# Kernel optimization log

Measured on AMD Instinct MI355X. Metric: run time of the kernel, lower is better.

The kernel has to match this reference:

```python
import jax, jax.numpy as jnp
import numpy as np

E = 2048      # embed_dim = qk_dim = v_dim = proj_dim
H = 16        # n_head
D = 128       # head_dim
ROT = 64      # rotary_dim (partial rotary: ROT < D)
PAD = 50257   # pad_token_id in select_at_last_token
EPS = 1e-5    # layer_norm_epsilon


def _sincos(T):
    # fixed_pos_embedding (GPT-J style): [T, ROT//2] each
    inv_freq = 1.0 / (10000.0 ** (jnp.arange(0, ROT, 2, dtype=jnp.float32) / ROT))
    ang = jnp.arange(T, dtype=jnp.float32)[:, None] * inv_freq[None, :]
    return jnp.sin(ang), jnp.cos(ang)


def _rope(x, sin, cos):
    # x: [B,T,H,ROT]; sin/cos: [T, ROT//2]; repeat_interleave(2) on last dim
    sin2 = jnp.repeat(sin, 2, axis=-1)[None, :, None, :]
    cos2 = jnp.repeat(cos, 2, axis=-1)[None, :, None, :]
    x1 = x[..., ::2]
    x2 = x[..., 1::2]
    rot = jnp.stack((-x2, x1), axis=-1).reshape(x.shape)  # rotate_every_two
    return x * cos2 + rot * sin2


def setup_inputs() -> dict:
    key = jax.random.key(0)
    ks = jax.random.split(key, 8)
    B, S = 8, 2048
    s = 0.02
    return {
        "hidden_states": jax.random.normal(ks[0], (B, S, E), jnp.float32),
        "input_ids_with_pads": jax.random.randint(ks[1], (B, S), 0, PAD),
        "ln_w": jnp.ones((E,), jnp.float32),
        "ln_b": jnp.zeros((E,), jnp.float32),
        "q_w": jax.random.normal(ks[2], (E, E), jnp.float32) * s,
        "q_b": jnp.zeros((E,), jnp.float32),
        "k_w": jax.random.normal(ks[3], (E, E), jnp.float32) * s,
        "k_b": jnp.zeros((E,), jnp.float32),
        "v_w": jax.random.normal(ks[4], (E, E), jnp.float32) * s,
        "v_b": jnp.zeros((E,), jnp.float32),
        "out_w": jax.random.normal(ks[5], (E, E), jnp.float32) * s,
        "out_b": jnp.zeros((E,), jnp.float32),
    }


def reference(hidden_states, input_ids_with_pads, ln_w, ln_b,
              q_w, q_b, k_w, k_b, v_w, v_b, out_w, out_b):
    B, S, _ = hidden_states.shape
    # LayerNorm
    mu = jnp.mean(hidden_states, axis=-1, keepdims=True)
    var = jnp.mean(jnp.square(hidden_states - mu), axis=-1, keepdims=True)
    hs = (hidden_states - mu) * jax.lax.rsqrt(var + EPS) * ln_w + ln_b
    # select_at_last_token: index of last non-pad token per row
    ix = jnp.argmax(jnp.cumsum((input_ids_with_pads != PAD).astype(jnp.int32), axis=1), axis=1)  # [B]
    h_last = jnp.take_along_axis(hs, ix[:, None, None], axis=1)  # [B,1,E]
    # projections (pool_to_vector: single query token)
    q = h_last @ q_w.T + q_b           # [B,1,E]
    k = hs @ k_w.T + k_b               # [B,S,E]
    v = hs @ v_w.T + v_b               # [B,S,E]
    # split heads; rotary layout keeps [B,T,H,D] for q,k
    q = q.reshape(B, 1, H, D)
    k = k.reshape(B, S, H, D)
    v = v.reshape(B, S, H, D).transpose(0, 2, 1, 3)  # [B,H,S,D]
    # partial rotary on first ROT dims (query at position 0, keys 0..S-1)
    sin, cos = _sincos(S)
    q = jnp.concatenate([_rope(q[..., :ROT], sin[:1], cos[:1]), q[..., ROT:]], axis=-1)
    k = jnp.concatenate([_rope(k[..., :ROT], sin, cos), k[..., ROT:]], axis=-1)
    q = q.transpose(0, 2, 1, 3)  # [B,H,1,D]
    k = k.transpose(0, 2, 1, 3)  # [B,H,S,D]
    # GPT-Neo _attn: no 1/sqrt(d) scaling; `bias` buffer is all-ones so the
    # causal mask is all-True and masked_bias is never applied.
    scores = jnp.einsum('bhqd,bhkd->bhqk', q, k)   # [B,H,1,S]
    attn = jax.nn.softmax(scores, axis=-1)
    out = jnp.einsum('bhqk,bhkd->bhqd', attn, v)   # [B,H,1,D]
    out = out.transpose(0, 2, 1, 3).reshape(B, 1, H * D)  # merge heads
    out = out @ out_w.T + out_b                    # out_proj
    return out[:, 0, :]                            # squeeze(-2): [B,E]
```

## Files before the change

### kernel.cpp

```cpp
#include <hip/hip_runtime.h>
#include <hip/hip_bf16.h>
#include <cstdint>
#include <cstddef>


using bf16x8 = __attribute__((ext_vector_type(8))) __bf16;
using f32x4  = __attribute__((ext_vector_type(4))) float;

__device__ __forceinline__ unsigned short f2bf(float f) {
  unsigned u = __float_as_uint(f);
  u += 0x7fffu + ((u >> 16) & 1u);
  return (unsigned short)(u >> 16);
}

__device__ __forceinline__ void gld16(const void* g, void* l) {
  __builtin_amdgcn_global_load_lds((__attribute__((address_space(1))) void*)g,
                                   (__attribute__((address_space(3))) void*)l,
                                   16, 0, 0);
}

#define FENCE() asm volatile("" ::: "memory")
#define SBAR()  { FENCE(); __builtin_amdgcn_s_barrier(); FENCE(); }
#define VM8()   asm volatile("s_waitcnt vmcnt(8)" ::: "memory")
#define VM0()   asm volatile("s_waitcnt vmcnt(0)" ::: "memory")

__global__ __launch_bounds__(256) void prep_kernel(
    const float* __restrict__ hidden, const int* __restrict__ ids,
    const float* __restrict__ gw, const float* __restrict__ gb,
    const float* __restrict__ kw, unsigned short* __restrict__ hs,
    unsigned short* __restrict__ Wk, float2* __restrict__ tab,
    float* __restrict__ hl, float* __restrict__ Z) {
  const int blk = blockIdx.x, tid = threadIdx.x;
  const int wave = tid >> 6, lane = tid & 63;

  if (blk < 16384) {
    const size_t row = blk;
    const float* xr = hidden + row * 2048;
    float4 a = ((const float4*)xr)[tid];
    float4 b = ((const float4*)xr)[tid + 256];
    float s  = a.x + a.y + a.z + a.w + b.x + b.y + b.z + b.w;
    float ss = a.x*a.x + a.y*a.y + a.z*a.z + a.w*a.w +
               b.x*b.x + b.y*b.y + b.z*b.z + b.w*b.w;
    for (int m = 1; m < 64; m <<= 1) { s += __shfl_xor(s, m); ss += __shfl_xor(ss, m); }
    __shared__ float rs[4], rss[4];
    if (lane == 0) { rs[wave] = s; rss[wave] = ss; }
    __syncthreads();
    s  = rs[0] + rs[1] + rs[2] + rs[3];
    ss = rss[0] + rss[1] + rss[2] + rss[3];
    const float mu = s * (1.f / 2048.f);
    const float var = ss * (1.f / 2048.f) - mu * mu;
    const float r = rsqrtf(var + 1e-5f);
    const int i0 = tid * 4, i1 = 1024 + tid * 4;
    ushort4 p0 = {f2bf((a.x - mu) * r * gw[i0 + 0] + gb[i0 + 0]),
                  f2bf((a.y - mu) * r * gw[i0 + 1] + gb[i0 + 1]),
                  f2bf((a.z - mu) * r * gw[i0 + 2] + gb[i0 + 2]),
                  f2bf((a.w - mu) * r * gw[i0 + 3] + gb[i0 + 3])};
    ushort4 p1 = {f2bf((b.x - mu) * r * gw[i1 + 0] + gb[i1 + 0]),
                  f2bf((b.y - mu) * r * gw[i1 + 1] + gb[i1 + 1]),
                  f2bf((b.z - mu) * r * gw[i1 + 2] + gb[i1 + 2]),
                  f2bf((b.w - mu) * r * gw[i1 + 3] + gb[i1 + 3])};
    *(ushort4*)(hs + row * 2048 + i0) = p0;
    *(ushort4*)(hs + row * 2048 + i1) = p1;
  } else if (blk < 18432) {
    const size_t i4 = (size_t)(blk - 16384) * 256 + tid;
    const int r = (int)(i4 >> 9);
    const int col4 = (int)(i4 & 511);
    const size_t src4 = ((size_t)((r >> 6) * 128 + (r & 63))) * 512 + col4;
    float4 v = ((const float4*)kw)[src4];
    ushort4 o = {f2bf(v.x), f2bf(v.y), f2bf(v.z), f2bf(v.w)};
    ((ushort4*)Wk)[i4] = o;
  } else if (blk < 18688) {
    const int t = (blk - 18432) * 8 + (tid >> 5);
    const int i = tid & 31;
    const float inv = exp2f(-(float)i * (13.287712379549449f / 32.f));
    const float ang = (float)t * inv;
    tab[t * 32 + i] = make_float2(sinf(ang), cosf(ang));
  } else {
    const int b = blk - 18688;
    if (tid < 16) Z[b * 16 + tid] = 0.f;
    int best = -1;
    for (int t = tid; t < 2048; t += 256)
      if (ids[b * 2048 + t] != 50257) best = (t > best) ? t : best;
    for (int m = 1; m < 64; m <<= 1) {
      int o = __shfl_xor(best, m);
      best = (o > best) ? o : best;
    }
    __shared__ int rb[4];
    if (lane == 0) rb[wave] = best;
    __syncthreads();
    int ix = rb[0];
    for (int w = 1; w < 4; ++w) ix = (rb[w] > ix) ? rb[w] : ix;
    ix = (ix < 0) ? 0 : ix;
    const float* xr = hidden + ((size_t)b * 2048 + ix) * 2048;
    float4 a = ((const float4*)xr)[tid];
    float4 c = ((const float4*)xr)[tid + 256];
    float s  = a.x + a.y + a.z + a.w + c.x + c.y + c.z + c.w;
    float ss = a.x*a.x + a.y*a.y + a.z*a.z + a.w*a.w +
               c.x*c.x + c.y*c.y + c.z*c.z + c.w*c.w;
    for (int m = 1; m < 64; m <<= 1) { s += __shfl_xor(s, m); ss += __shfl_xor(ss, m); }
    __shared__ float rs2[4], rss2[4];
    if (lane == 0) { rs2[wave] = s; rss2[wave] = ss; }
    __syncthreads();
    s  = rs2[0] + rs2[1] + rs2[2] + rs2[3];
    ss = rss2[0] + rss2[1] + rss2[2] + rss2[3];
    const float mu = s * (1.f / 2048.f);
    const float var = ss * (1.f / 2048.f) - mu * mu;
    const float r = rsqrtf(var + 1e-5f);
    const int i0 = tid * 4, i1 = 1024 + tid * 4;
    float* yo = hl + (size_t)b * 2048;
    yo[i0 + 0] = (a.x - mu) * r * gw[i0 + 0] + gb[i0 + 0];
    yo[i0 + 1] = (a.y - mu) * r * gw[i0 + 1] + gb[i0 + 1];
    yo[i0 + 2] = (a.z - mu) * r * gw[i0 + 2] + gb[i0 + 2];
    yo[i0 + 3] = (a.w - mu) * r * gw[i0 + 3] + gb[i0 + 3];
    yo[i1 + 0] = (c.x - mu) * r * gw[i1 + 0] + gb[i1 + 0];
    yo[i1 + 1] = (c.y - mu) * r * gw[i1 + 1] + gb[i1 + 1];
    yo[i1 + 2] = (c.z - mu) * r * gw[i1 + 2] + gb[i1 + 2];
    yo[i1 + 3] = (c.w - mu) * r * gw[i1 + 3] + gb[i1 + 3];
  }
}

__global__ __launch_bounds__(256) void gemv8_kernel(const float* __restrict__ X,
                                                    const float* __restrict__ W,
                                                    const float* __restrict__ bias,
                                                    float* __restrict__ Y) {
  const int tid = threadIdx.x, lane = tid & 63, wave = tid >> 6;
  const int e = blockIdx.x * 4 + wave;
  const float* wr = W + (size_t)e * 2048;
  float p[8] = {0, 0, 0, 0, 0, 0, 0, 0};
#pragma unroll
  for (int it = 0; it < 8; ++it) {
    const int k = it * 256 + lane * 4;
    float4 wv = *(const float4*)(wr + k);
#pragma unroll
    for (int b = 0; b < 8; ++b) {
      float4 xv = *(const float4*)(X + b * 2048 + k);
      p[b] += wv.x * xv.x + wv.y * xv.y + wv.z * xv.z + wv.w * xv.w;
    }
  }
#pragma unroll
  for (int b = 0; b < 8; ++b)
    for (int m = 1; m < 64; m <<= 1) p[b] += __shfl_xor(p[b], m);
  if (lane == 0) {
    const float bb = bias[e];
#pragma unroll
    for (int b = 0; b < 8; ++b) Y[(size_t)b * 2048 + e] = p[b] + bb;
  }
}

__global__ __launch_bounds__(256) void fold_c_kernel(
    const float* __restrict__ qv, const float* __restrict__ kw,
    const float* __restrict__ kb, unsigned short* __restrict__ Cpad,
    float* __restrict__ qkb) {
  const int bh = blockIdx.x, b = bh >> 4, h = bh & 15;
  const int tid = threadIdx.x;
  const float* qh = qv + ((size_t)b * 16 + h) * 128 + 64;
  const int e0 = tid * 8;
  float acc[8] = {0, 0, 0, 0, 0, 0, 0, 0};
  for (int c = 0; c < 64; ++c) {
    const float qc = qh[c];
    const float* row = kw + ((size_t)(h * 128 + 64 + c)) * 2048 + e0;
    float4 v0 = *(const float4*)(row);
    float4 v1 = *(const float4*)(row + 4);
    acc[0] += qc * v0.x; acc[1] += qc * v0.y; acc[2] += qc * v0.z; acc[3] += qc * v0.w;
    acc[4] += qc * v1.x; acc[5] += qc * v1.y; acc[6] += qc * v1.z; acc[7] += qc * v1.w;
  }
  unsigned short* dst = Cpad + ((size_t)b * 128 + h) * 2048 + e0;
  ushort4 o0 = {f2bf(acc[0]), f2bf(acc[1]), f2bf(acc[2]), f2bf(acc[3])};
  ushort4 o1 = {f2bf(acc[4]), f2bf(acc[5]), f2bf(acc[6]), f2bf(acc[7])};
  *(ushort4*)(dst) = o0;
  *(ushort4*)(dst + 4) = o1;
  if (tid < 64) {
    float p = kb[h * 128 + 64 + tid] * qh[tid];
    for (int m = 1; m < 64; m <<= 1) p += __shfl_xor(p, m);
    if (tid == 0) qkb[bh] = p;
  }
}

__global__ __launch_bounds__(256) void gemm_plain_kernel(
    const unsigned short* __restrict__ A, const unsigned short* __restrict__ Cpad,
    const float* __restrict__ qkb, float* __restrict__ spS) {
  constexpr int K = 2048;
  __shared__ unsigned short As[128 * 32];
  __shared__ unsigned short Bs[128 * 32];
  const int tid = threadIdx.x;
  const int lane = tid & 63, wave = tid >> 6;
  const int wr = wave >> 1, wc = wave & 1;
  const int bm = blockIdx.x;
  const int b = bm >> 4;

  const unsigned short* Ap = A + ((size_t)(bm * 128 + (tid >> 2))) * K + (tid & 3) * 8;
  const unsigned short* Bp = Cpad + ((size_t)b * 128 + (tid >> 2)) * K + (tid & 3) * 8;
  unsigned short* lA0 = As + wave * 512;
  unsigned short* lA1 = As + 2048 + wave * 512;
  unsigned short* lB0 = Bs + wave * 512;
  unsigned short* lB1 = Bs + 2048 + wave * 512;

  f32x4 acc[4][4];
#pragma unroll
  for (int i = 0; i < 4; ++i)
#pragma unroll
    for (int j = 0; j < 4; ++j) acc[i][j] = (f32x4){0.f, 0.f, 0.f, 0.f};

  const unsigned short* aPtr[4];
  const unsigned short* bPtr[4];
#pragma unroll
  for (int mi = 0; mi < 4; ++mi)
    aPtr[mi] = As + (wr * 64 + mi * 16 + (lane & 15)) * 32 + (lane >> 4) * 8;
#pragma unroll
  for (int ni = 0; ni < 4; ++ni)
    bPtr[ni] = Bs + (wc * 64 + ni * 16 + (lane & 15)) * 32 + (lane >> 4) * 8;

  for (int kt = 0; kt < K / 32; ++kt) {
    const int ko = kt * 32;
    gld16(Ap + ko,          lA0);
    gld16(Ap + ko + 64 * K, lA1);
    gld16(Bp + ko,          lB0);
    gld16(Bp + ko + 64 * K, lB1);
    __syncthreads();
    bf16x8 af[4], bfr[4];
#pragma unroll
    for (int mi = 0; mi < 4; ++mi) af[mi] = *(const bf16x8*)aPtr[mi];
#pragma unroll
    for (int ni = 0; ni < 4; ++ni) bfr[ni] = *(const bf16x8*)bPtr[ni];
#pragma unroll
    for (int mi = 0; mi < 4; ++mi)
#pragma unroll
      for (int ni = 0; ni < 4; ++ni)
        acc[mi][ni] = __builtin_amdgcn_mfma_f32_16x16x32_bf16(af[mi], bfr[ni],
                                                              acc[mi][ni], 0, 0, 0);
    __syncthreads();
  }

  if (wc == 0) {
    const int rg = lane >> 4, l15 = lane & 15;
    const float qk = qkb[b * 16 + l15];
#pragma unroll
    for (int mi = 0; mi < 4; ++mi)
#pragma unroll
      for (int r = 0; r < 4; ++r) {
        const int row = wr * 64 + mi * 16 + rg * 4 + r;
        spS[((size_t)bm * 128 + row) * 16 + l15] = acc[mi][0][r] + qk;
      }
  }
}

__global__ __launch_bounds__(512, 2) void gemm_kscore_rot_kernel(
    const unsigned short* __restrict__ A, const unsigned short* __restrict__ W,
    const float* __restrict__ kb, const float* __restrict__ qv,
    const float2* __restrict__ tab, const float* __restrict__ spS,
    float* __restrict__ sw_t, float* __restrict__ Z) {
  constexpr int K = 2048;
  constexpr int NT = K / 64;
  __shared__ unsigned short Ls[4 * 16384];

  const int tid = threadIdx.x;
  const int lane = tid & 63, wave = tid >> 6;
  const int wr = wave >> 2, wc = wave & 3;
  const int l15 = lane & 15, lk = lane >> 4, l7 = lane & 7;

  const int orig = blockIdx.x;
  const int wgid = (orig & 7) * 32 + (orig >> 3);
  const int bm = wgid >> 2;
  const int bn = wgid & 3;

  const int srow = tid >> 3;
  const int scb  = (tid & 7) ^ (srow & 7);
  const unsigned short* Asrc = A + ((size_t)(bm * 256 + srow)) * K + scb * 8;
  const unsigned short* Bsrc = W + ((size_t)(bn * 256 + srow)) * K + scb * 8;
  const int wave512 = wave * 512;

  f32x4 acc[8][4];
#pragma unroll
  for (int i = 0; i < 8; ++i)
#pragma unroll
    for (int j = 0; j < 4; ++j) acc[i][j] = (f32x4){0.f, 0.f, 0.f, 0.f};

  int rowA[8], rowB[4];
#pragma unroll
  for (int mi = 0; mi < 8; ++mi) rowA[mi] = (wr * 128 + mi * 16 + l15) * 64;
#pragma unroll
  for (int nj = 0; nj < 4; ++nj) rowB[nj] = (wc * 64 + nj * 16 + l15) * 64;

#pragma unroll
  for (int p = 0; p < 4; ++p) {
    gld16(Asrc + (size_t)p * 64 * K, Ls + p * 4096 + wave512);
    gld16(Bsrc + (size_t)p * 64 * K, Ls + 16384 + p * 4096 + wave512);
  }
#pragma unroll
  for (int p = 0; p < 4; ++p) {
    gld16(Asrc + (size_t)p * 64 * K + 64, Ls + 32768 + p * 4096 + wave512);
    gld16(Bsrc + (size_t)p * 64 * K + 64, Ls + 49152 + p * 4096 + wave512);
  }
  VM8();
  SBAR();

  for (int t = 0; t < NT; ++t) {
    const unsigned short* bufA = Ls + (t & 1) * 32768;
    const unsigned short* bufB = bufA + 16384;
#pragma unroll
    for (int ks = 0; ks < 2; ++ks) {
      const int offk = ((((ks << 2) | lk) ^ l7) << 3);
      bf16x8 af[8], bfr[4];
#pragma unroll
      for (int mi = 0; mi < 8; ++mi)
        af[mi] = *(const bf16x8*)(bufA + rowA[mi] + offk);
#pragma unroll
      for (int nj = 0; nj < 4; ++nj)
        bfr[nj] = *(const bf16x8*)(bufB + rowB[nj] + offk);
#pragma unroll
      for (int mi = 0; mi < 8; ++mi)
#pragma unroll
        for (int nj = 0; nj < 4; ++nj)
          acc[mi][nj] = __builtin_amdgcn_mfma_f32_16x16x32_bf16(
              af[mi], bfr[nj], acc[mi][nj], 0, 0, 0);
    }
    if (t == NT - 1) break;
    SBAR();
    if (t + 2 < NT) {
      const int k0 = (t + 2) * 64;
      unsigned short* dA = Ls + (t & 1) * 32768 + wave512;
      unsigned short* dB = dA + 16384;
#pragma unroll
      for (int p = 0; p < 4; ++p) {
        gld16(Asrc + (size_t)p * 64 * K + k0, dA + p * 4096);
        gld16(Bsrc + (size_t)p * 64 * K + k0, dB + p * 4096);
      }
      VM8();
    } else {
      VM0();
    }
    SBAR();
  }

  const int b  = bm >> 3;
  const int h  = bn * 4 + wc;
  const int rg = lk;
  const float* qb  = qv + ((size_t)b * 16 + h) * 128;
  const float* kbh = kb + h * 128;
  float rowsum[8][4];
#pragma unroll
  for (int mi = 0; mi < 8; ++mi)
#pragma unroll
    for (int r = 0; r < 4; ++r) rowsum[mi][r] = 0.f;

  const int s0g = bm * 256 + wr * 128;
  const float sgn = (l15 & 1) ? -1.f : 1.f;
#pragma unroll
  for (int nj = 0; nj < 4; ++nj) {
    const int c = nj * 16 + l15;
    const float qd   = qb[c];
    const float qps  = sgn * qb[c ^ 1];
    const float bias = kbh[c];
    const int i = c >> 1;
#pragma unroll
    for (int mi = 0; mi < 8; ++mi)
#pragma unroll
      for (int r = 0; r < 4; ++r) {
        const int t = s0g + mi * 16 + rg * 4 + r;
        const float2 sc = tab[(t & 2047) * 32 + i];
        rowsum[mi][r] += (acc[mi][nj][r] + bias) * (qd * sc.y + qps * sc.x);
      }
  }
#pragma unroll
  for (int mi = 0; mi < 8; ++mi)
#pragma unroll
    for (int r = 0; r < 4; ++r) {
      float v = rowsum[mi][r];
      v += __shfl_xor(v, 1);
      v += __shfl_xor(v, 2);
      v += __shfl_xor(v, 4);
      v += __shfl_xor(v, 8);
      rowsum[mi][r] = v;
    }
  float zpart = 0.f;
  if (l15 == 0) {
#pragma unroll
    for (int mi = 0; mi < 8; ++mi)
#pragma unroll
      for (int r = 0; r < 4; ++r) {
        const int gr = s0g + mi * 16 + rg * 4 + r;
        const float sc = rowsum[mi][r] + spS[(size_t)gr * 16 + h];
        const float w = __expf(sc - 40.f);
        sw_t[(size_t)gr * 16 + h] = w;
        zpart += w;
      }
    zpart += __shfl_xor(zpart, 16);
    zpart += __shfl_xor(zpart, 32);
    if (lane == 0) atomicAdd(&Z[b * 16 + h], zpart);
  }
}

__global__ __launch_bounds__(256) void attn_wsum_kernel(
    const unsigned short* __restrict__ hs, const float* __restrict__ sw_t,
    float* __restrict__ part) {
  const int b = blockIdx.x, ech = blockIdx.y, tc = blockIdx.z;
  const int tid = threadIdx.x;
  const int e = ech * 512 + tid * 2;
  __shared__ float sw[128 * 16];
  {
    const float4* src = (const float4*)(sw_t + ((size_t)b * 2048 + tc * 128) * 16);
    float4* dst = (float4*)sw;
    dst[tid] = src[tid];
    dst[tid + 256] = src[tid + 256];
  }
  __syncthreads();
  float a0[16], a1[16];
#pragma unroll
  for (int h = 0; h < 16; ++h) { a0[h] = 0.f; a1[h] = 0.f; }
  const unsigned short* hp = hs + ((size_t)b * 2048 + tc * 128) * 2048 + e;
#pragma unroll 2
  for (int tt = 0; tt < 128; ++tt) {
    const unsigned hv = *(const unsigned*)(hp + (size_t)tt * 2048);
    const float h0 = __uint_as_float(hv << 16);
    const float h1 = __uint_as_float(hv & 0xffff0000u);
    const float4 w0 = *(const float4*)(sw + tt * 16 + 0);
    const float4 w1 = *(const float4*)(sw + tt * 16 + 4);
    const float4 w2 = *(const float4*)(sw + tt * 16 + 8);
    const float4 w3 = *(const float4*)(sw + tt * 16 + 12);
    const float wv[16] = {w0.x, w0.y, w0.z, w0.w, w1.x, w1.y, w1.z, w1.w,
                          w2.x, w2.y, w2.z, w2.w, w3.x, w3.y, w3.z, w3.w};
#pragma unroll
    for (int h = 0; h < 16; ++h) {
      a0[h] += wv[h] * h0;
      a1[h] += wv[h] * h1;
    }
  }
#pragma unroll
  for (int h = 0; h < 16; ++h) {
    float2 st = {a0[h], a1[h]};
    *(float2*)(part + (((size_t)tc * 8 + b) * 16 + h) * 2048 + e) = st;
  }
}

__global__ __launch_bounds__(256) void attn_comb_kernel(
    const float* __restrict__ part, const float* __restrict__ Z,
    float* __restrict__ wsumN) {
  const int bh = blockIdx.x, b = bh >> 4, h = bh & 15;
  const float zi = 1.f / Z[bh];
  for (int e = threadIdx.x; e < 2048; e += 256) {
    float s = 0.f;
#pragma unroll
    for (int tc = 0; tc < 16; ++tc)
      s += part[(((size_t)tc * 8 + b) * 16 + h) * 2048 + e];
    wsumN[(size_t)bh * 2048 + e] = s * zi;
  }
}

__global__ __launch_bounds__(256) void attn_vgemv_kernel(
    const float* __restrict__ vw, const float* __restrict__ vb,
    const float* __restrict__ wsumN, float* __restrict__ aout) {
  const int tid = threadIdx.x, lane = tid & 63, wave = tid >> 6;
  const int gw = blockIdx.x * 4 + wave;
  const int h = gw >> 7, d = gw & 127;
  const float* vr = vw + (size_t)gw * 2048;
  float p[8] = {0, 0, 0, 0, 0, 0, 0, 0};
#pragma unroll
  for (int it = 0; it < 8; ++it) {
    const int k = it * 256 + lane * 4;
    float4 wv = *(const float4*)(vr + k);
#pragma unroll
    for (int b = 0; b < 8; ++b) {
      float4 xv = *(const float4*)(wsumN + ((size_t)b * 16 + h) * 2048 + k);
      p[b] += wv.x * xv.x + wv.y * xv.y + wv.z * xv.z + wv.w * xv.w;
    }
  }
#pragma unroll
  for (int b = 0; b < 8; ++b)
    for (int m = 1; m < 64; m <<= 1) p[b] += __shfl_xor(p[b], m);
  if (lane == 0) {
    const float bb = vb[gw];
#pragma unroll
    for (int b = 0; b < 8; ++b)
      aout[((size_t)b * 16 + h) * 128 + d] = p[b] + bb;
  }
}

extern "C" void kernel_launch(void* const* d_in, const int* in_sizes, int n_in,
                              void* d_out, int out_size, void* d_ws, size_t ws_size,
                              hipStream_t stream) {
  (void)in_sizes; (void)n_in; (void)out_size; (void)ws_size;
  const float* hidden = (const float*)d_in[0];
  const int*   ids    = (const int*)d_in[1];
  const float* ln_w   = (const float*)d_in[2];
  const float* ln_b   = (const float*)d_in[3];
  const float* q_w    = (const float*)d_in[4];
  const float* q_b    = (const float*)d_in[5];
  const float* k_w    = (const float*)d_in[6];
  const float* k_b    = (const float*)d_in[7];
  const float* v_w    = (const float*)d_in[8];
  const float* v_b    = (const float*)d_in[9];
  const float* out_w  = (const float*)d_in[10];
  const float* out_b  = (const float*)d_in[11];
  float* out = (float*)d_out;

  char* ws = (char*)d_ws;
  unsigned short* hs  = (unsigned short*)ws; ws += (size_t)16384 * 2048 * 2;
  unsigned short* Wk  = (unsigned short*)ws; ws += (size_t)1024 * 2048 * 2;
  unsigned short* Cpad = (unsigned short*)ws; ws += (size_t)8 * 128 * 2048 * 2;
  float2* sctab = (float2*)ws; ws += (size_t)2048 * 32 * 8;
  float* qv     = (float*)ws; ws += (size_t)8 * 2048 * 4;
  float* hl     = (float*)ws; ws += (size_t)8 * 2048 * 4;
  float* aout   = (float*)ws; ws += (size_t)8 * 2048 * 4;
  float* sw_t   = (float*)ws; ws += (size_t)8 * 2048 * 16 * 4;
  float* spS    = (float*)ws; ws += (size_t)16384 * 16 * 4;
  float* qkb    = (float*)ws; ws += 128 * 4;
  float* Zb     = (float*)ws; ws += 128 * 4;
  float* part   = (float*)ws; ws += (size_t)16 * 8 * 16 * 2048 * 4;
  float* wsumN  = (float*)ws; ws += (size_t)128 * 2048 * 4;

  prep_kernel<<<18696, 256, 0, stream>>>(hidden, ids, ln_w, ln_b, k_w,
                                         hs, Wk, sctab, hl, Zb);
  gemv8_kernel<<<512, 256, 0, stream>>>(hl, q_w, q_b, qv);
  fold_c_kernel<<<128, 256, 0, stream>>>(qv, k_w, k_b, Cpad, qkb);
  gemm_plain_kernel<<<128, 256, 0, stream>>>(hs, Cpad, qkb, spS);
  gemm_kscore_rot_kernel<<<256, 512, 0, stream>>>(hs, Wk, k_b, qv,
                                                  sctab, spS, sw_t, Zb);
  attn_wsum_kernel<<<dim3(8, 4, 16), 256, 0, stream>>>(hs, sw_t, part);
  attn_comb_kernel<<<128, 256, 0, stream>>>(part, Zb, wsumN);
  attn_vgemv_kernel<<<512, 256, 0, stream>>>(v_w, v_b, wsumN, aout);
  gemv8_kernel<<<512, 256, 0, stream>>>(aout, out_w, out_b, out);
}
```

Baseline: 441.5 us.

## Fuse plain-score GEMM into rotary K-score GEMM, removing separate kernel and spS buffer

Removes the separate gemm_plain_kernel that computed the non-rotary part of the attention scores against the folded query matrix. Its work is folded into the main K-score GEMM: each block also streams a small slice of Cpad into LDS and runs one extra MFMA per row tile, then adds the result to the rotary row sums through a lane shuffle. This avoids a second full pass over the 64 MB bf16 hidden-state matrix, one launch, and the spS round trip through global memory. In exchange it adds LDS use, accumulator registers and an asymmetric wait count in wave 0, and it uses setprio around the MFMA block.

```diff
diff --git a/kernel.cpp b/kernel.cpp
--- a/kernel.cpp
+++ b/kernel.cpp
@@ -21,6 +21,7 @@
 
 #define FENCE() asm volatile("" ::: "memory")
 #define SBAR()  { FENCE(); __builtin_amdgcn_s_barrier(); FENCE(); }
+#define VM9()   asm volatile("s_waitcnt vmcnt(9)" ::: "memory")
 #define VM8()   asm volatile("s_waitcnt vmcnt(8)" ::: "memory")
 #define VM0()   asm volatile("s_waitcnt vmcnt(0)" ::: "memory")
 
@@ -176,82 +177,15 @@
   }
 }
 
-__global__ __launch_bounds__(256) void gemm_plain_kernel(
-    const unsigned short* __restrict__ A, const unsigned short* __restrict__ Cpad,
-    const float* __restrict__ qkb, float* __restrict__ spS) {
-  constexpr int K = 2048;
-  __shared__ unsigned short As[128 * 32];
-  __shared__ unsigned short Bs[128 * 32];
-  const int tid = threadIdx.x;
-  const int lane = tid & 63, wave = tid >> 6;
-  const int wr = wave >> 1, wc = wave & 1;
-  const int bm = blockIdx.x;
-  const int b = bm >> 4;
-
-  const unsigned short* Ap = A + ((size_t)(bm * 128 + (tid >> 2))) * K + (tid & 3) * 8;
-  const unsigned short* Bp = Cpad + ((size_t)b * 128 + (tid >> 2)) * K + (tid & 3) * 8;
-  unsigned short* lA0 = As + wave * 512;
-  unsigned short* lA1 = As + 2048 + wave * 512;
-  unsigned short* lB0 = Bs + wave * 512;
-  unsigned short* lB1 = Bs + 2048 + wave * 512;
-
-  f32x4 acc[4][4];
-#pragma unroll
-  for (int i = 0; i < 4; ++i)
-#pragma unroll
-    for (int j = 0; j < 4; ++j) acc[i][j] = (f32x4){0.f, 0.f, 0.f, 0.f};
-
-  const unsigned short* aPtr[4];
-  const unsigned short* bPtr[4];
-#pragma unroll
-  for (int mi = 0; mi < 4; ++mi)
-    aPtr[mi] = As + (wr * 64 + mi * 16 + (lane & 15)) * 32 + (lane >> 4) * 8;
-#pragma unroll
-  for (int ni = 0; ni < 4; ++ni)
-    bPtr[ni] = Bs + (wc * 64 + ni * 16 + (lane & 15)) * 32 + (lane >> 4) * 8;
-
-  for (int kt = 0; kt < K / 32; ++kt) {
-    const int ko = kt * 32;
-    gld16(Ap + ko,          lA0);
-    gld16(Ap + ko + 64 * K, lA1);
-    gld16(Bp + ko,          lB0);
-    gld16(Bp + ko + 64 * K, lB1);
-    __syncthreads();
-    bf16x8 af[4], bfr[4];
-#pragma unroll
-    for (int mi = 0; mi < 4; ++mi) af[mi] = *(const bf16x8*)aPtr[mi];
-#pragma unroll
-    for (int ni = 0; ni < 4; ++ni) bfr[ni] = *(const bf16x8*)bPtr[ni];
-#pragma unroll
-    for (int mi = 0; mi < 4; ++mi)
-#pragma unroll
-      for (int ni = 0; ni < 4; ++ni)
-        acc[mi][ni] = __builtin_amdgcn_mfma_f32_16x16x32_bf16(af[mi], bfr[ni],
-                                                              acc[mi][ni], 0, 0, 0);
-    __syncthreads();
-  }
-
-  if (wc == 0) {
-    const int rg = lane >> 4, l15 = lane & 15;
-    const float qk = qkb[b * 16 + l15];
-#pragma unroll
-    for (int mi = 0; mi < 4; ++mi)
-#pragma unroll
-      for (int r = 0; r < 4; ++r) {
-        const int row = wr * 64 + mi * 16 + rg * 4 + r;
-        spS[((size_t)bm * 128 + row) * 16 + l15] = acc[mi][0][r] + qk;
-      }
-  }
-}
-
 __global__ __launch_bounds__(512, 2) void gemm_kscore_rot_kernel(
     const unsigned short* __restrict__ A, const unsigned short* __restrict__ W,
+    const unsigned short* __restrict__ Cpad, const float* __restrict__ qkb,
     const float* __restrict__ kb, const float* __restrict__ qv,
-    const float2* __restrict__ tab, const float* __restrict__ spS,
-    float* __restrict__ sw_t, float* __restrict__ Z) {
+    const float2* __restrict__ tab, float* __restrict__ sw_t,
+    float* __restrict__ Z) {
   constexpr int K = 2048;
   constexpr int NT = K / 64;
-  __shared__ unsigned short Ls[4 * 16384];
+  __shared__ unsigned short Ls[4 * 16384 + 2 * 1024];
 
   const int tid = threadIdx.x;
   const int lane = tid & 63, wave = tid >> 6;
@@ -262,57 +196,76 @@
   const int wgid = (orig & 7) * 32 + (orig >> 3);
   const int bm = wgid >> 2;
   const int bn = wgid & 3;
+  const int b  = bm >> 3;
 
   const int srow = tid >> 3;
   const int scb  = (tid & 7) ^ (srow & 7);
   const unsigned short* Asrc = A + ((size_t)(bm * 256 + srow)) * K + scb * 8;
   const unsigned short* Bsrc = W + ((size_t)(bn * 256 + srow)) * K + scb * 8;
+  const int crow = (lane >> 3) & 3;
+  const int ccb  = (lane & 7) ^ (crow & 7);
+  const unsigned short* Csrc =
+      Cpad + ((size_t)(b * 128 + bn * 4 + crow)) * K + ccb * 8;
   const int wave512 = wave * 512;
+  unsigned short* Lc = Ls + 65536;
 
   f32x4 acc[8][4];
-#pragma unroll
-  for (int i = 0; i < 8; ++i)
+  f32x4 accc[8];
+#pragma unroll
+  for (int i = 0; i < 8; ++i) {
+    accc[i] = (f32x4){0.f, 0.f, 0.f, 0.f};
 #pragma unroll
     for (int j = 0; j < 4; ++j) acc[i][j] = (f32x4){0.f, 0.f, 0.f, 0.f};
+  }
 
   int rowA[8], rowB[4];
 #pragma unroll
   for (int mi = 0; mi < 8; ++mi) rowA[mi] = (wr * 128 + mi * 16 + l15) * 64;
 #pragma unroll
   for (int nj = 0; nj < 4; ++nj) rowB[nj] = (wc * 64 + nj * 16 + l15) * 64;
+  const int rowC = l15 * 64;
 
 #pragma unroll
   for (int p = 0; p < 4; ++p) {
     gld16(Asrc + (size_t)p * 64 * K, Ls + p * 4096 + wave512);
     gld16(Bsrc + (size_t)p * 64 * K, Ls + 16384 + p * 4096 + wave512);
   }
+  if (wave == 0 && lane < 32) gld16(Csrc, Lc);
 #pragma unroll
   for (int p = 0; p < 4; ++p) {
     gld16(Asrc + (size_t)p * 64 * K + 64, Ls + 32768 + p * 4096 + wave512);
     gld16(Bsrc + (size_t)p * 64 * K + 64, Ls + 49152 + p * 4096 + wave512);
   }
-  VM8();
+  if (wave == 0 && lane < 32) gld16(Csrc + 64, Lc + 1024);
+  if (wave == 0) { VM9(); } else { VM8(); }
   SBAR();
 
   for (int t = 0; t < NT; ++t) {
     const unsigned short* bufA = Ls + (t & 1) * 32768;
     const unsigned short* bufB = bufA + 16384;
+    const unsigned short* bufC = Lc + (t & 1) * 1024;
 #pragma unroll
     for (int ks = 0; ks < 2; ++ks) {
       const int offk = ((((ks << 2) | lk) ^ l7) << 3);
-      bf16x8 af[8], bfr[4];
+      bf16x8 af[8], bfr[4], cf;
 #pragma unroll
       for (int mi = 0; mi < 8; ++mi)
         af[mi] = *(const bf16x8*)(bufA + rowA[mi] + offk);
 #pragma unroll
       for (int nj = 0; nj < 4; ++nj)
         bfr[nj] = *(const bf16x8*)(bufB + rowB[nj] + offk);
-#pragma unroll
-      for (int mi = 0; mi < 8; ++mi)
+      cf = *(const bf16x8*)(bufC + rowC + offk);
+      __builtin_amdgcn_s_setprio(1);
+#pragma unroll
+      for (int mi = 0; mi < 8; ++mi) {
+        accc[mi] = __builtin_amdgcn_mfma_f32_16x16x32_bf16(af[mi], cf,
+                                                           accc[mi], 0, 0, 0);
 #pragma unroll
         for (int nj = 0; nj < 4; ++nj)
           acc[mi][nj] = __builtin_amdgcn_mfma_f32_16x16x32_bf16(
               af[mi], bfr[nj], acc[mi][nj], 0, 0, 0);
+      }
+      __builtin_amdgcn_s_setprio(0);
     }
     if (t == NT - 1) break;
     SBAR();
@@ -325,18 +278,19 @@
         gld16(Asrc + (size_t)p * 64 * K + k0, dA + p * 4096);
         gld16(Bsrc + (size_t)p * 64 * K + k0, dB + p * 4096);
       }
-      VM8();
+      if (wave == 0 && lane < 32) gld16(Csrc + k0, Lc + (t & 1) * 1024);
+      if (wave == 0) { VM9(); } else { VM8(); }
     } else {
       VM0();
     }
     SBAR();
   }
 
-  const int b  = bm >> 3;
   const int h  = bn * 4 + wc;
   const int rg = lk;
   const float* qb  = qv + ((size_t)b * 16 + h) * 128;
   const float* kbh = kb + h * 128;
+  const float qkbv = qkb[b * 16 + h];
   float rowsum[8][4];
 #pragma unroll
   for (int mi = 0; mi < 8; ++mi)
@@ -372,6 +326,13 @@
       v += __shfl_xor(v, 8);
       rowsum[mi][r] = v;
     }
+  const int srcl = (lane & 48) | wc;
+#pragma unroll
+  for (int mi = 0; mi < 8; ++mi)
+#pragma unroll
+    for (int r = 0; r < 4; ++r)
+      rowsum[mi][r] += __shfl(accc[mi][r], srcl) + qkbv;
+
   float zpart = 0.f;
   if (l15 == 0) {
 #pragma unroll
@@ -379,8 +340,7 @@
 #pragma unroll
       for (int r = 0; r < 4; ++r) {
         const int gr = s0g + mi * 16 + rg * 4 + r;
-        const float sc = rowsum[mi][r] + spS[(size_t)gr * 16 + h];
-        const float w = __expf(sc - 40.f);
+        const float w = __expf(rowsum[mi][r] - 40.f);
         sw_t[(size_t)gr * 16 + h] = w;
         zpart += w;
       }
@@ -502,7 +462,6 @@
   float* hl     = (float*)ws; ws += (size_t)8 * 2048 * 4;
   float* aout   = (float*)ws; ws += (size_t)8 * 2048 * 4;
   float* sw_t   = (float*)ws; ws += (size_t)8 * 2048 * 16 * 4;
-  float* spS    = (float*)ws; ws += (size_t)16384 * 16 * 4;
   float* qkb    = (float*)ws; ws += 128 * 4;
   float* Zb     = (float*)ws; ws += 128 * 4;
   float* part   = (float*)ws; ws += (size_t)16 * 8 * 16 * 2048 * 4;
@@ -512,11 +471,10 @@
                                          hs, Wk, sctab, hl, Zb);
   gemv8_kernel<<<512, 256, 0, stream>>>(hl, q_w, q_b, qv);
   fold_c_kernel<<<128, 256, 0, stream>>>(qv, k_w, k_b, Cpad, qkb);
-  gemm_plain_kernel<<<128, 256, 0, stream>>>(hs, Cpad, qkb, spS);
-  gemm_kscore_rot_kernel<<<256, 512, 0, stream>>>(hs, Wk, k_b, qv,
-                                                  sctab, spS, sw_t, Zb);
+  gemm_kscore_rot_kernel<<<256, 512, 0, stream>>>(hs, Wk, Cpad, qkb, k_b, qv,
+                                                  sctab, sw_t, Zb);
   attn_wsum_kernel<<<dim3(8, 4, 16), 256, 0, stream>>>(hs, sw_t, part);
   attn_comb_kernel<<<128, 256, 0, stream>>>(part, Zb, wsumN);
-  attn_vgemv_kernel<<<512, 256, 0, stream>>>(v_w, v_b, wsumN, aout);
+  attn_vgemv_kernel<<<512, 256, 0, stream>>>(v_b ? v_w : v_w, v_b, wsumN, aout);
   gemv8_kernel<<<512, 256, 0, stream>>>(aout, out_w, out_b, out);
 }
```

New measurement: 401.2 us. 9.1% less time.
